# Optimization experiments

Measured on AMD Instinct MI355X. Metric: run time of the kernel, lower is better.

The kernel has to match this reference:

```python
import jax, jax.numpy as jnp
import numpy as np

S, B, E, H = 2048, 2, 1024, 16
D = E // H  # head_dim = 64


def setup_inputs() -> dict:
    key = jax.random.key(0)
    ks = jax.random.split(key, 11)
    std = 1.0 / np.sqrt(E)
    return {
        "query": jax.random.normal(ks[0], (S, B, E), jnp.float32),
        "key": jax.random.normal(ks[1], (S, B, E), jnp.float32),
        "value": jax.random.normal(ks[2], (S, B, E), jnp.float32),
        "q_w": jax.random.uniform(ks[3], (E, E), jnp.float32, -std, std),
        "q_b": jax.random.uniform(ks[4], (E,), jnp.float32, -std, std),
        "k_w": jax.random.uniform(ks[5], (E, E), jnp.float32, -std, std),
        "k_b": jax.random.uniform(ks[6], (E,), jnp.float32, -std, std),
        "v_w": jax.random.uniform(ks[7], (E, E), jnp.float32, -std, std),
        "v_b": jax.random.uniform(ks[8], (E,), jnp.float32, -std, std),
        "out_w": jax.random.uniform(ks[9], (E, E), jnp.float32, -std, std),
        "out_b": jax.random.uniform(ks[10], (E,), jnp.float32, -std, std),
    }


def reference(query, key, value, q_w, q_b, k_w, k_b, v_w, v_b, out_w, out_b):
    tgt_len, bsz, embed_dim = query.shape
    src_len = key.shape[0]
    head_dim = embed_dim // H
    scaling = head_dim ** -0.5

    # nn.Linear: x @ W.T + b
    q = (jnp.einsum('sbe,fe->sbf', query, q_w) + q_b) * scaling
    k = jnp.einsum('sbe,fe->sbf', key, k_w) + k_b
    v = jnp.einsum('sbe,fe->sbf', value, v_w) + v_b

    # [S, B, E] -> [B*H, S, D]
    def split_heads(x, n):
        return x.reshape(n, bsz * H, head_dim).transpose(1, 0, 2)

    q = split_heads(q, tgt_len)
    k = split_heads(k, src_len)
    v = split_heads(v, src_len)

    scores = jnp.einsum('bqd,bkd->bqk', q, k)        # [B*H, S, S]
    attn = jax.nn.softmax(scores, axis=-1)            # dropout p=0 -> identity
    out = jnp.einsum('bqk,bkd->bqd', attn, v)         # [B*H, S, D]
    out = out.transpose(1, 0, 2).reshape(tgt_len, bsz, embed_dim)
    Z = jnp.einsum('sbe,fe->sbf', out, out_w) + out_b
    attn_avg = attn.reshape(bsz, H, tgt_len, src_len).sum(axis=1) / H
    return Z, attn_avg
```

## Files before the change

### kernel.cpp

```cpp
#include <hip/hip_runtime.h>
#include <hip/hip_fp16.h>
#include <cstdint>
#include <cstddef>

#define S_LEN 2048
#define BATCH 2
#define EMB   1024
#define NHEAD 16
#define HDIM  64

typedef short short8 __attribute__((ext_vector_type(8)));
typedef float f32x4  __attribute__((ext_vector_type(4)));

__device__ __forceinline__ unsigned short f2b(float f) {
    unsigned int u = __float_as_uint(f);
    u = (u + 0x7FFFu + ((u >> 16) & 1u)) >> 16;
    return (unsigned short)u;
}
__device__ __forceinline__ unsigned int pk2(float a, float b) {
    return (unsigned int)f2b(a) | ((unsigned int)f2b(b) << 16);
}
__device__ __forceinline__ float b2f_lo(unsigned int u) { return __uint_as_float(u << 16); }
__device__ __forceinline__ float b2f_hi(unsigned int u) { return __uint_as_float(u & 0xFFFF0000u); }

__device__ __forceinline__ void gload_lds16(const ushort* g, ushort* l) {
    __builtin_amdgcn_global_load_lds(
        (const __attribute__((address_space(1))) void*)g,
        (__attribute__((address_space(3))) void*)l, 16, 0, 0);
}

__global__ __launch_bounds__(256)
void cast3(const float* __restrict__ s0, const float* __restrict__ s1,
           const float* __restrict__ s2, ushort* __restrict__ d0,
           ushort* __restrict__ d1, ushort* __restrict__ d2)
{
    const float* s = (blockIdx.y == 0) ? s0 : (blockIdx.y == 1) ? s1 : s2;
    ushort*      d = (blockIdx.y == 0) ? d0 : (blockIdx.y == 1) ? d1 : d2;
    const size_t i = ((size_t)blockIdx.x * 256 + threadIdx.x) * 8;
    const float4 a = *(const float4*)(s + i);
    const float4 b = *(const float4*)(s + i + 4);
    *(uint4*)(d + i) = make_uint4(pk2(a.x, a.y), pk2(a.z, a.w),
                                  pk2(b.x, b.y), pk2(b.z, b.w));
}

__global__ __launch_bounds__(256)
void cast4(const float* __restrict__ s0, const float* __restrict__ s1,
           const float* __restrict__ s2, const float* __restrict__ s3,
           ushort* __restrict__ d0, ushort* __restrict__ d1,
           ushort* __restrict__ d2, ushort* __restrict__ d3)
{
    const float* s = (blockIdx.y == 0) ? s0 : (blockIdx.y == 1) ? s1
                   : (blockIdx.y == 2) ? s2 : s3;
    ushort*      d = (blockIdx.y == 0) ? d0 : (blockIdx.y == 1) ? d1
                   : (blockIdx.y == 2) ? d2 : d3;
    const size_t i = ((size_t)blockIdx.x * 256 + threadIdx.x) * 8;
    const float4 a = *(const float4*)(s + i);
    const float4 b = *(const float4*)(s + i + 4);
    *(uint4*)(d + i) = make_uint4(pk2(a.x, a.y), pk2(a.z, a.w),
                                  pk2(b.x, b.y), pk2(b.z, b.w));
}

__device__ __forceinline__ void gemm_core(
    ushort (*As)[128 * 32], ushort (*Bs)[128 * 32],
    const ushort* __restrict__ A, const ushort* __restrict__ W,
    const float* __restrict__ bias, void* __restrict__ out_,
    float scale, int mode)
{
    constexpr int K  = EMB;
    constexpr int NT = K / 32;

    const int t    = threadIdx.x;
    const int lane = t & 63;
    const int wave = t >> 6;
    const int quad = lane >> 4;
    const int l15  = lane & 15;
    const int wm   = wave >> 2;
    const int wn   = wave & 3;
    const int m0   = blockIdx.x * 128;
    const int n0   = blockIdx.y * 128;

    const int srow = t >> 2;
    const int sseg = ((t & 3) ^ ((srow >> 1) & 3)) << 3;
    const ushort* gA = A + (size_t)(m0 + srow) * K + sseg;
    const ushort* gW = W + (size_t)(n0 + srow) * K + sseg;

    f32x4 acc[4][2];
#pragma unroll
    for (int mi = 0; mi < 4; ++mi)
#pragma unroll
        for (int ni = 0; ni < 2; ++ni) acc[mi][ni] = (f32x4){0.f, 0.f, 0.f, 0.f};

#define STAGE(buf, kt) do {                         \
        gload_lds16(gA + (kt) * 32, &As[buf][t * 8]); \
        gload_lds16(gW + (kt) * 32, &Bs[buf][t * 8]); \
    } while (0)

    STAGE(0, 0);
    __syncthreads();

    for (int kt = 0; kt < NT; ++kt) {
        const int cur = kt & 1;
        if (kt + 1 < NT) STAGE(cur ^ 1, kt + 1);
        short8 af[4], bf[2];
#pragma unroll
        for (int mi = 0; mi < 4; ++mi) {
            const int ra = wm * 64 + mi * 16 + l15;
            af[mi] = *(const short8*)&As[cur][ra * 32 + ((quad ^ ((ra >> 1) & 3)) << 3)];
        }
#pragma unroll
        for (int ni = 0; ni < 2; ++ni) {
            const int rb = wn * 32 + ni * 16 + l15;
            bf[ni] = *(const short8*)&Bs[cur][rb * 32 + ((quad ^ ((rb >> 1) & 3)) << 3)];
        }
#pragma unroll
        for (int mi = 0; mi < 4; ++mi)
#pragma unroll
            for (int ni = 0; ni < 2; ++ni)
                acc[mi][ni] = __builtin_amdgcn_mfma_f32_16x16x32_bf16(
                    af[mi], bf[ni], acc[mi][ni], 0, 0, 0);
        __syncthreads();
    }
#undef STAGE

#pragma unroll
    for (int mi = 0; mi < 4; ++mi)
#pragma unroll
        for (int ni = 0; ni < 2; ++ni) {
            const int col = n0 + wn * 32 + ni * 16 + l15;
            const float bc = bias[col];
#pragma unroll
            for (int r = 0; r < 4; ++r) {
                const int rg = m0 + wm * 64 + mi * 16 + quad * 4 + r;
                const float v = (acc[mi][ni][r] + bc) * scale;
                if (mode == 0) {
                    ((float*)out_)[(size_t)rg * EMB + col] = v;
                } else {
                    const int s  = rg >> 1;
                    const int bb = rg & 1;
                    const int h  = col >> 6;
                    const int d  = col & 63;
                    if (mode == 1)
                        ((ushort*)out_)[(((size_t)(bb * NHEAD + h)) * S_LEN + s) * HDIM + d] = f2b(v);
                    else
                        ((ushort*)out_)[(((size_t)(bb * NHEAD + h)) * HDIM + d) * S_LEN + s] = f2b(v);
                }
            }
        }
}

__global__ __launch_bounds__(512, 2)
void gemm_qkv(const ushort* __restrict__ qi, const ushort* __restrict__ ki,
              const ushort* __restrict__ vi,
              const ushort* __restrict__ qW, const ushort* __restrict__ kW,
              const ushort* __restrict__ vW,
              const float* __restrict__ qB, const float* __restrict__ kB,
              const float* __restrict__ vB,
              ushort* __restrict__ qO, ushort* __restrict__ kO,
              ushort* __restrict__ vO)
{
    __shared__ ushort As[2][128 * 32];
    __shared__ ushort Bs[2][128 * 32];
    const int z = blockIdx.z;
    const ushort* A    = (z == 0) ? qi : (z == 1) ? ki : vi;
    const ushort* W    = (z == 0) ? qW : (z == 1) ? kW : vW;
    const float* bias  = (z == 0) ? qB : (z == 1) ? kB : vB;
    ushort* out        = (z == 0) ? qO : (z == 1) ? kO : vO;
    const float scale  = (z == 0) ? 0.125f : 1.0f;
    const int   mode   = (z == 2) ? 2 : 1;
    gemm_core(As, Bs, A, W, bias, out, scale, mode);
}

__global__ __launch_bounds__(512, 2)
void gemm_z(const ushort* __restrict__ A, const ushort* __restrict__ W,
            const float* __restrict__ bias, float* __restrict__ out)
{
    __shared__ ushort As[2][128 * 32];
    __shared__ ushort Bs[2][128 * 32];
    gemm_core(As, Bs, A, W, bias, out, 1.0f, 0);
}

#define PLD 2056
__global__ __launch_bounds__(512, 2)
void attn_bf16(const ushort* __restrict__ qw, const ushort* __restrict__ kw,
               const ushort* __restrict__ vt, ushort* __restrict__ ao,
               ushort* __restrict__ pavg_ws)
{
    __shared__ ushort pLds[16 * PLD];
    __shared__ float  redS[8 * 16];
    __shared__ float  red2[4 * 16 * 16];

    const int t     = threadIdx.x;
    const int lane  = t & 63;
    const int wave  = t >> 6;
    const int quad  = lane >> 4;
    const int l15   = lane & 15;
    const int rbase = quad * 4;

    const int bid     = blockIdx.x;
    const int logical = (bid & 7) * 64 + (bid >> 3);
    const int qt      = logical & 127;
    const int rest    = logical >> 7;
    const int b       = rest & 1;
    const int g       = rest >> 1;
    const int sq0     = qt * 16;

    const int ntile = wave & 3;
    const int khalf = wave >> 2;
    const int colAvg = (wave * 16 + l15) * 16;

    __half2 pavg[4][8];
#pragma unroll
    for (int r = 0; r < 4; ++r)
#pragma unroll
        for (int j = 0; j < 8; ++j) pavg[r][j] = __float2half2_rn(0.f);

    for (int hh = 0; hh < 8; ++hh) {
        const int h  = g * 8 + hh;
        const int bh = b * NHEAD + h;
        const ushort* qbase = qw + ((size_t)bh * S_LEN + sq0) * HDIM;
        const ushort* kbse  = kw + (size_t)bh * S_LEN * HDIM;

        const short8 qf0 = *(const short8*)(qbase + l15 * HDIM + quad * 8);
        const short8 qf1 = *(const short8*)(qbase + l15 * HDIM + 32 + quad * 8);

        float s4[4] = {0.f, 0.f, 0.f, 0.f};
#pragma unroll
        for (int ti = 0; ti < 16; ++ti) {
            const int c0 = wave * 256 + ti * 16;
            const ushort* kr = kbse + (size_t)(c0 + l15) * HDIM;
            const short8 k0 = *(const short8*)(kr + quad * 8);
            const short8 k1 = *(const short8*)(kr + 32 + quad * 8);
            f32x4 a = (f32x4){0.f, 0.f, 0.f, 0.f};
            a = __builtin_amdgcn_mfma_f32_16x16x32_bf16(qf0, k0, a, 0, 0, 0);
            a = __builtin_amdgcn_mfma_f32_16x16x32_bf16(qf1, k1, a, 0, 0, 0);
#pragma unroll
            for (int r = 0; r < 4; ++r) {
                const float e = exp2f(fmaf(a[r], 1.44269504f, -11.54156035f));
                s4[r] += e;
                pLds[(rbase + r) * PLD + c0 + l15] = f2b(e);
            }
        }
#pragma unroll
        for (int off = 1; off < 16; off <<= 1)
#pragma unroll
            for (int r = 0; r < 4; ++r) s4[r] += __shfl_xor(s4[r], off, 16);
        if (l15 == 0)
#pragma unroll
            for (int r = 0; r < 4; ++r) redS[wave * 16 + rbase + r] = s4[r];
        __syncthreads();

        float rinv[4];
#pragma unroll
        for (int r = 0; r < 4; ++r) {
            float s = redS[rbase + r];
#pragma unroll
            for (int w = 1; w < 8; ++w) s += redS[w * 16 + rbase + r];
            rinv[r] = 1.0f / s;
        }

#pragma unroll
        for (int r = 0; r < 4; ++r) {
            const __half2 hri2 = __float2half2_rn(rinv[r]);
#pragma unroll
            for (int c = 0; c < 2; ++c) {
                const uint4 u = *(const uint4*)&pLds[(rbase + r) * PLD + colAvg + c * 8];
                pavg[r][c*4+0] = __hfma2(__floats2half2_rn(b2f_lo(u.x), b2f_hi(u.x)), hri2, pavg[r][c*4+0]);
                pavg[r][c*4+1] = __hfma2(__floats2half2_rn(b2f_lo(u.y), b2f_hi(u.y)), hri2, pavg[r][c*4+1]);
                pavg[r][c*4+2] = __hfma2(__floats2half2_rn(b2f_lo(u.z), b2f_hi(u.z)), hri2, pavg[r][c*4+2]);
                pavg[r][c*4+3] = __hfma2(__floats2half2_rn(b2f_lo(u.w), b2f_hi(u.w)), hri2, pavg[r][c*4+3]);
            }
        }

        const ushort* vrow = vt + ((size_t)bh * HDIM + ntile * 16 + l15) * S_LEN + khalf * 1024;
        const ushort* prow = &pLds[l15 * PLD + khalf * 1024];
        f32x4 o0 = (f32x4){0.f, 0.f, 0.f, 0.f}, o1 = o0;
#pragma unroll
        for (int st = 0; st < 32; st += 2) {
            const short8 pa0 = *(const short8*)(prow + st * 32 + quad * 8);
            const short8 vb0 = *(const short8*)(vrow + st * 32 + quad * 8);
            o0 = __builtin_amdgcn_mfma_f32_16x16x32_bf16(pa0, vb0, o0, 0, 0, 0);
            const short8 pa1 = *(const short8*)(prow + (st + 1) * 32 + quad * 8);
            const short8 vb1 = *(const short8*)(vrow + (st + 1) * 32 + quad * 8);
            o1 = __builtin_amdgcn_mfma_f32_16x16x32_bf16(pa1, vb1, o1, 0, 0, 0);
        }
        const f32x4 o = o0 + o1;
        if (khalf == 1) {
#pragma unroll
            for (int r = 0; r < 4; ++r)
                red2[ntile * 256 + (rbase + r) * 16 + l15] = o[r];
        }
        __syncthreads();
        if (khalf == 0) {
#pragma unroll
            for (int r = 0; r < 4; ++r) {
                const float val = (o[r] + red2[ntile * 256 + (rbase + r) * 16 + l15]) * rinv[r];
                const int s = sq0 + rbase + r;
                const int d = ntile * 16 + l15;
                ao[((size_t)s * BATCH + b) * EMB + h * HDIM + d] = f2b(val);
            }
        }
    }

    const float inv16 = 0.0625f;
#pragma unroll
    for (int r = 0; r < 4; ++r) {
        const int s = sq0 + rbase + r;
        ushort* dst = pavg_ws + (((size_t)(g * BATCH + b)) * S_LEN + s) * S_LEN + colAvg;
#pragma unroll
        for (int c = 0; c < 2; ++c) {
            const float2 f0 = __half22float2(pavg[r][c*4+0]);
            const float2 f1 = __half22float2(pavg[r][c*4+1]);
            const float2 f2 = __half22float2(pavg[r][c*4+2]);
            const float2 f3 = __half22float2(pavg[r][c*4+3]);
            uint4 u;
            u.x = pk2(f0.x * inv16, f0.y * inv16);
            u.y = pk2(f1.x * inv16, f1.y * inv16);
            u.z = pk2(f2.x * inv16, f2.y * inv16);
            u.w = pk2(f3.x * inv16, f3.y * inv16);
            *(uint4*)(dst + c * 8) = u;
        }
    }
}

__global__ __launch_bounds__(256)
void avg_reduce(const ushort* __restrict__ p, float* __restrict__ out)
{
    const size_t N = (size_t)BATCH * S_LEN * S_LEN;
    const size_t i = ((size_t)blockIdx.x * 256 + threadIdx.x) * 8;
    const uint4 a = *(const uint4*)(p + i);
    const uint4 c = *(const uint4*)(p + i + N);
    float4 o0 = make_float4(b2f_lo(a.x) + b2f_lo(c.x), b2f_hi(a.x) + b2f_hi(c.x),
                            b2f_lo(a.y) + b2f_lo(c.y), b2f_hi(a.y) + b2f_hi(c.y));
    float4 o1 = make_float4(b2f_lo(a.z) + b2f_lo(c.z), b2f_hi(a.z) + b2f_hi(c.z),
                            b2f_lo(a.w) + b2f_lo(c.w), b2f_hi(a.w) + b2f_hi(c.w));
    *(float4*)(out + i)     = o0;
    *(float4*)(out + i + 4) = o1;
}

extern "C" void kernel_launch(void* const* d_in, const int* in_sizes, int n_in,
                              void* d_out, int out_size, void* d_ws, size_t ws_size,
                              hipStream_t stream)
{
    const float* query = (const float*)d_in[0];
    const float* key   = (const float*)d_in[1];
    const float* value = (const float*)d_in[2];
    const float* q_w   = (const float*)d_in[3];
    const float* q_b   = (const float*)d_in[4];
    const float* k_w   = (const float*)d_in[5];
    const float* k_b   = (const float*)d_in[6];
    const float* v_w   = (const float*)d_in[7];
    const float* v_b   = (const float*)d_in[8];
    const float* out_w = (const float*)d_in[9];
    const float* out_b = (const float*)d_in[10];

    float* Z        = (float*)d_out;
    float* attn_avg = Z + (size_t)S_LEN * BATCH * EMB;

    const size_t QKV = (size_t)S_LEN * BATCH * EMB;
    ushort* q_ws    = (ushort*)d_ws;
    ushort* k_ws    = q_ws + QKV;
    ushort* vt_ws   = k_ws + QKV;
    ushort* ao_ws   = vt_ws + QKV;
    ushort* pavg_ws = ao_ws + QKV;
    ushort* qbf     = pavg_ws + 2 * (size_t)BATCH * S_LEN * S_LEN;
    ushort* kbf     = qbf + QKV;
    ushort* vbf     = kbf + QKV;
    ushort* wqb     = vbf + QKV;
    ushort* wkb     = wqb + (size_t)EMB * EMB;
    ushort* wvb     = wkb + (size_t)EMB * EMB;
    ushort* wob     = wvb + (size_t)EMB * EMB;

    cast3<<<dim3(2048, 3), 256, 0, stream>>>(query, key, value, qbf, kbf, vbf);
    cast4<<<dim3(512, 4), 256, 0, stream>>>(q_w, k_w, v_w, out_w, wqb, wkb, wvb, wob);

    const dim3 blkG(512);
    const dim3 gq(32, 8, 3);
    gemm_qkv<<<gq, blkG, 0, stream>>>(qbf, kbf, vbf, wqb, wkb, wvb,
                                      q_b, k_b, v_b, q_ws, k_ws, vt_ws);

    attn_bf16<<<dim3(512), dim3(512), 0, stream>>>(q_ws, k_ws, vt_ws, ao_ws, pavg_ws);

    avg_reduce<<<4096, 256, 0, stream>>>(pavg_ws, attn_avg);

    const dim3 gz(32, 8);
    gemm_z<<<gz, blkG, 0, stream>>>(ao_ws, wob, out_b, Z);
}
```

Baseline: 454.4 us.

## Recompute head-averaged attention probabilities in a separate kernel from saved row inverses

New measurement: 518.1 us. 1.14x slower.

```diff
diff --git a/kernel.cpp b/kernel.cpp
--- a/kernel.cpp
+++ b/kernel.cpp
@@ -180,10 +180,10 @@
 }
 
 #define PLD 2056
-__global__ __launch_bounds__(512, 2)
+__global__ __launch_bounds__(512, 4)
 void attn_bf16(const ushort* __restrict__ qw, const ushort* __restrict__ kw,
                const ushort* __restrict__ vt, ushort* __restrict__ ao,
-               ushort* __restrict__ pavg_ws)
+               float* __restrict__ rinv_ws)
 {
     __shared__ ushort pLds[16 * PLD];
     __shared__ float  redS[8 * 16];
@@ -206,13 +206,6 @@
 
     const int ntile = wave & 3;
     const int khalf = wave >> 2;
-    const int colAvg = (wave * 16 + l15) * 16;
-
-    __half2 pavg[4][8];
-#pragma unroll
-    for (int r = 0; r < 4; ++r)
-#pragma unroll
-        for (int j = 0; j < 8; ++j) pavg[r][j] = __float2half2_rn(0.f);
 
     for (int hh = 0; hh < 8; ++hh) {
         const int h  = g * 8 + hh;
@@ -257,18 +250,10 @@
             for (int w = 1; w < 8; ++w) s += redS[w * 16 + rbase + r];
             rinv[r] = 1.0f / s;
         }
-
-#pragma unroll
-        for (int r = 0; r < 4; ++r) {
-            const __half2 hri2 = __float2half2_rn(rinv[r]);
-#pragma unroll
-            for (int c = 0; c < 2; ++c) {
-                const uint4 u = *(const uint4*)&pLds[(rbase + r) * PLD + colAvg + c * 8];
-                pavg[r][c*4+0] = __hfma2(__floats2half2_rn(b2f_lo(u.x), b2f_hi(u.x)), hri2, pavg[r][c*4+0]);
-                pavg[r][c*4+1] = __hfma2(__floats2half2_rn(b2f_lo(u.y), b2f_hi(u.y)), hri2, pavg[r][c*4+1]);
-                pavg[r][c*4+2] = __hfma2(__floats2half2_rn(b2f_lo(u.z), b2f_hi(u.z)), hri2, pavg[r][c*4+2]);
-                pavg[r][c*4+3] = __hfma2(__floats2half2_rn(b2f_lo(u.w), b2f_hi(u.w)), hri2, pavg[r][c*4+3]);
-            }
+        if (wave == 0 && l15 == 0) {
+#pragma unroll
+            for (int r = 0; r < 4; ++r)
+                rinv_ws[(size_t)bh * S_LEN + sq0 + rbase + r] = rinv[r];
         }
 
         const ushort* vrow = vt + ((size_t)bh * HDIM + ntile * 16 + l15) * S_LEN + khalf * 1024;
@@ -300,41 +285,74 @@
             }
         }
     }
+}
+
+__global__ __launch_bounds__(512, 2)
+void pavg_scores(const ushort* __restrict__ qw, const ushort* __restrict__ kw,
+                 const float* __restrict__ rinv_ws, float* __restrict__ out)
+{
+    const int t     = threadIdx.x;
+    const int lane  = t & 63;
+    const int wave  = t >> 6;
+    const int quad  = lane >> 4;
+    const int l15   = lane & 15;
+    const int rbase = quad * 4;
+
+    const int bid     = blockIdx.x;
+    const int logical = (bid & 7) * 64 + (bid >> 3);
+    const int kc      = logical >> 6;
+    const int b       = (logical >> 5) & 1;
+    const int sqc     = logical & 31;
+
+    const int k0row = kc * 256 + wave * 32;
+
+    float pacc[4][2][4];
+#pragma unroll
+    for (int s4i = 0; s4i < 4; ++s4i)
+#pragma unroll
+        for (int t2 = 0; t2 < 2; ++t2)
+#pragma unroll
+            for (int r = 0; r < 4; ++r) pacc[s4i][t2][r] = 0.f;
+
+    for (int h = 0; h < NHEAD; ++h) {
+        const int bh = b * NHEAD + h;
+        const ushort* kr0 = kw + ((size_t)bh * S_LEN + k0row + l15) * HDIM;
+        const ushort* kr1 = kw + ((size_t)bh * S_LEN + k0row + 16 + l15) * HDIM;
+        const short8 kf00 = *(const short8*)(kr0 + quad * 8);
+        const short8 kf01 = *(const short8*)(kr0 + 32 + quad * 8);
+        const short8 kf10 = *(const short8*)(kr1 + quad * 8);
+        const short8 kf11 = *(const short8*)(kr1 + 32 + quad * 8);
+        const float* rbse = rinv_ws + (size_t)bh * S_LEN + sqc * 64;
+#pragma unroll
+        for (int s4i = 0; s4i < 4; ++s4i) {
+            const ushort* qbase = qw + ((size_t)bh * S_LEN + sqc * 64 + s4i * 16) * HDIM;
+            const short8 qf0 = *(const short8*)(qbase + l15 * HDIM + quad * 8);
+            const short8 qf1 = *(const short8*)(qbase + l15 * HDIM + 32 + quad * 8);
+            f32x4 a0 = (f32x4){0.f, 0.f, 0.f, 0.f}, a1 = a0;
+            a0 = __builtin_amdgcn_mfma_f32_16x16x32_bf16(qf0, kf00, a0, 0, 0, 0);
+            a0 = __builtin_amdgcn_mfma_f32_16x16x32_bf16(qf1, kf01, a0, 0, 0, 0);
+            a1 = __builtin_amdgcn_mfma_f32_16x16x32_bf16(qf0, kf10, a1, 0, 0, 0);
+            a1 = __builtin_amdgcn_mfma_f32_16x16x32_bf16(qf1, kf11, a1, 0, 0, 0);
+#pragma unroll
+            for (int r = 0; r < 4; ++r) {
+                const float ri = rbse[s4i * 16 + rbase + r];
+                pacc[s4i][0][r] = fmaf(exp2f(fmaf(a0[r], 1.44269504f, -11.54156035f)), ri, pacc[s4i][0][r]);
+                pacc[s4i][1][r] = fmaf(exp2f(fmaf(a1[r], 1.44269504f, -11.54156035f)), ri, pacc[s4i][1][r]);
+            }
+        }
+    }
 
     const float inv16 = 0.0625f;
 #pragma unroll
-    for (int r = 0; r < 4; ++r) {
-        const int s = sq0 + rbase + r;
-        ushort* dst = pavg_ws + (((size_t)(g * BATCH + b)) * S_LEN + s) * S_LEN + colAvg;
-#pragma unroll
-        for (int c = 0; c < 2; ++c) {
-            const float2 f0 = __half22float2(pavg[r][c*4+0]);
-            const float2 f1 = __half22float2(pavg[r][c*4+1]);
-            const float2 f2 = __half22float2(pavg[r][c*4+2]);
-            const float2 f3 = __half22float2(pavg[r][c*4+3]);
-            uint4 u;
-            u.x = pk2(f0.x * inv16, f0.y * inv16);
-            u.y = pk2(f1.x * inv16, f1.y * inv16);
-            u.z = pk2(f2.x * inv16, f2.y * inv16);
-            u.w = pk2(f3.x * inv16, f3.y * inv16);
-            *(uint4*)(dst + c * 8) = u;
-        }
-    }
-}
-
-__global__ __launch_bounds__(256)
-void avg_reduce(const ushort* __restrict__ p, float* __restrict__ out)
-{
-    const size_t N = (size_t)BATCH * S_LEN * S_LEN;
-    const size_t i = ((size_t)blockIdx.x * 256 + threadIdx.x) * 8;
-    const uint4 a = *(const uint4*)(p + i);
-    const uint4 c = *(const uint4*)(p + i + N);
-    float4 o0 = make_float4(b2f_lo(a.x) + b2f_lo(c.x), b2f_hi(a.x) + b2f_hi(c.x),
-                            b2f_lo(a.y) + b2f_lo(c.y), b2f_hi(a.y) + b2f_hi(c.y));
-    float4 o1 = make_float4(b2f_lo(a.z) + b2f_lo(c.z), b2f_hi(a.z) + b2f_hi(c.z),
-                            b2f_lo(a.w) + b2f_lo(c.w), b2f_hi(a.w) + b2f_hi(c.w));
-    *(float4*)(out + i)     = o0;
-    *(float4*)(out + i + 4) = o1;
+    for (int s4i = 0; s4i < 4; ++s4i)
+#pragma unroll
+        for (int t2 = 0; t2 < 2; ++t2)
+#pragma unroll
+            for (int r = 0; r < 4; ++r) {
+                const int sq = sqc * 64 + s4i * 16 + rbase + r;
+                const int sk = k0row + t2 * 16 + l15;
+                out[((size_t)b * S_LEN + sq) * S_LEN + sk] = pacc[s4i][t2][r] * inv16;
+            }
 }
 
 extern "C" void kernel_launch(void* const* d_in, const int* in_sizes, int n_in,
@@ -361,8 +379,8 @@
     ushort* k_ws    = q_ws + QKV;
     ushort* vt_ws   = k_ws + QKV;
     ushort* ao_ws   = vt_ws + QKV;
-    ushort* pavg_ws = ao_ws + QKV;
-    ushort* qbf     = pavg_ws + 2 * (size_t)BATCH * S_LEN * S_LEN;
+    float*  rinv_ws = (float*)(ao_ws + QKV);
+    ushort* qbf     = (ushort*)(rinv_ws + (size_t)BATCH * NHEAD * S_LEN);
     ushort* kbf     = qbf + QKV;
     ushort* vbf     = kbf + QKV;
     ushort* wqb     = vbf + QKV;
@@ -378,10 +396,10 @@
     gemm_qkv<<<gq, blkG, 0, stream>>>(qbf, kbf, vbf, wqb, wkb, wvb,
                                       q_b, k_b, v_b, q_ws, k_ws, vt_ws);
 
-    attn_bf16<<<dim3(512), dim3(512), 0, stream>>>(q_ws, k_ws, vt_ws, ao_ws, pavg_ws);
-
-    avg_reduce<<<4096, 256, 0, stream>>>(pavg_ws, attn_avg);
+    attn_bf16<<<dim3(512), dim3(512), 0, stream>>>(q_ws, k_ws, vt_ws, ao_ws, rinv_ws);
 
     const dim3 gz(32, 8);
     gemm_z<<<gz, blkG, 0, stream>>>(ao_ws, wob, out_b, Z);
-}
+
+    pavg_scores<<<dim3(512), dim3(512), 0, stream>>>(q_ws, k_ws, rinv_ws, attn_avg);
+}
```
